# Performance work log

Measured on AMD Instinct MI355X. Metric: run time of the kernel, lower is better.

The kernel has to match this reference:

```python
import jax, jax.numpy as jnp
import numpy as np

B, S, HID = 2, 2048, 2560
H, NOPE, ROPE, VD = 40, 64, 32, 64
QKD = NOPE + ROPE  # 96
Q_RANK, KV_RANK = 768, 256
EPS = 1e-5
SCALING = QKD ** -0.5
NEG = -1e9


def rms_norm(x, w, eps=EPS):
    xf = x.astype(jnp.float32)
    var = jnp.mean(xf * xf, axis=-1, keepdims=True)
    return (xf * jax.lax.rsqrt(var + eps)).astype(x.dtype) * w


def rotate_half(x):
    x1, x2 = jnp.split(x, 2, axis=-1)
    return jnp.concatenate([-x2, x1], axis=-1)


def setup_inputs() -> dict:
    key = jax.random.key(0)
    ks = jax.random.split(key, 8)
    # rotary tables (rope_theta = 10000), shape [S, ROPE]
    inv_freq = 1.0 / (10000.0 ** (np.arange(0, ROPE, 2, dtype=np.float32) / ROPE))
    t = np.arange(S, dtype=np.float32)
    freqs = np.outer(t, inv_freq)  # [S, ROPE/2]
    emb = np.concatenate([freqs, freqs], axis=-1)
    return {
        "hidden_states": jax.random.normal(ks[0], (B, S, HID), jnp.float32),
        "cos": jnp.asarray(np.cos(emb)),
        "sin": jnp.asarray(np.sin(emb)),
        "wq_a": jax.random.normal(ks[1], (HID, Q_RANK), jnp.float32) * 0.02,
        "q_a_ln_w": jnp.ones((Q_RANK,), jnp.float32),
        "wq_b": jax.random.normal(ks[2], (Q_RANK, H * QKD), jnp.float32) * 0.02,
        "wkv_a": jax.random.normal(ks[3], (HID, KV_RANK + ROPE), jnp.float32) * 0.02,
        "kv_a_ln_w": jnp.ones((KV_RANK,), jnp.float32),
        "wkv_b": jax.random.normal(ks[4], (KV_RANK, H * (NOPE + VD)), jnp.float32) * 0.02,
        "wo": jax.random.normal(ks[5], (H * VD, HID), jnp.float32) * 0.02,
    }


def reference(hidden_states, cos, sin, wq_a, q_a_ln_w, wq_b, wkv_a, kv_a_ln_w, wkv_b, wo):
    b, s, _ = hidden_states.shape
    # low-rank query: down-proj, RMSNorm, up-proj
    q = rms_norm(hidden_states @ wq_a, q_a_ln_w) @ wq_b  # [B,S,H*QKD]
    q = q.reshape(b, s, H, QKD).transpose(0, 2, 1, 3)  # [B,H,S,QKD]
    q_pass, q_rot = q[..., :NOPE], q[..., NOPE:]
    # compressed kv + shared rope key
    ckv = hidden_states @ wkv_a  # [B,S,KV_RANK+ROPE]
    k_c, k_rot = ckv[..., :KV_RANK], ckv[..., KV_RANK:]
    kv = rms_norm(k_c, kv_a_ln_w) @ wkv_b  # [B,S,H*(NOPE+VD)]
    kv = kv.reshape(b, s, H, NOPE + VD).transpose(0, 2, 1, 3)  # [B,H,S,NOPE+VD]
    k_pass, v = kv[..., :NOPE], kv[..., NOPE:]
    # partial RoPE (standard rotate-half), cos/sin: [S,ROPE] -> [1,1,S,ROPE]
    c = cos[None, None, :, :]
    si = sin[None, None, :, :]
    q_rot = q_rot * c + rotate_half(q_rot) * si  # [B,H,S,ROPE]
    k_rot = k_rot[:, None, :, :]  # [B,1,S,ROPE]
    k_rot = k_rot * c + rotate_half(k_rot) * si
    k_rot = jnp.broadcast_to(k_rot, (b, H, s, ROPE))
    query = jnp.concatenate([q_pass, q_rot], axis=-1)  # [B,H,S,QKD]
    key = jnp.concatenate([k_pass, k_rot], axis=-1)  # [B,H,S,QKD]
    # eager causal SDPA
    scores = jnp.einsum('bhqd,bhkd->bhqk', query, key) * SCALING
    causal = jnp.tril(jnp.ones((s, s), bool))
    scores = jnp.where(causal[None, None], scores, NEG)
    probs = jax.nn.softmax(scores.astype(jnp.float32), axis=-1).astype(query.dtype)
    out = jnp.einsum('bhqk,bhkd->bhqd', probs, v)  # [B,H,S,VD]
    out = out.transpose(0, 2, 1, 3).reshape(b, s, H * VD)
    return out @ wo
```

## Files before the change

### kernel.cpp

```cpp
#include <hip/hip_runtime.h>
#include <hip/hip_bf16.h>
#include <cstdint>

#define B_ 2
#define S_ 2048
#define HID_ 2560
#define H_ 40
#define NOPE_ 64
#define ROPE_ 32
#define VD_ 64
#define QKD_ 96
#define QRANK_ 768
#define KVRANK_ 256
#define KVRP_ 288
#define KVRP_PAD 384
#define HQKD (H_*QKD_)
#define HKV  (H_*(NOPE_+VD_))
#define HVD  (H_*VD_)
#define TOK  (B_*S_)
#define EPS_ 1e-5f
#define SCALING_ 0.10206207261596575f

typedef __bf16  bf16x8  __attribute__((ext_vector_type(8)));
typedef float   floatx4 __attribute__((ext_vector_type(4)));
typedef short   shortx4 __attribute__((ext_vector_type(4)));
typedef unsigned short ushort8_t __attribute__((ext_vector_type(8)));

__device__ __forceinline__ unsigned short f2bf(float f) {
    unsigned int u = __builtin_bit_cast(unsigned int, f);
    unsigned int r = (u + 0x7FFFu + ((u >> 16) & 1u)) >> 16;
    return (unsigned short)r;
}
__device__ __forceinline__ float bf2f(unsigned short h) {
    return __builtin_bit_cast(float, ((unsigned int)h) << 16);
}
__device__ __forceinline__ float load_in(const void* p, long i, int bf) {
    if (bf) return bf2f(((const unsigned short*)p)[i]);
    return ((const float*)p)[i];
}

__global__ void k_detect(const unsigned short* cosb, int* flag) {
    if (threadIdx.x == 0) flag[0] = (cosb[0] != 0) ? 1 : 0;
}

__global__ void k_tobf(const void* in, unsigned short* out, long n, const int* flag) {
    int bf = flag[0];
    long i = (long)blockIdx.x * blockDim.x + threadIdx.x;
    if (i >= n) return;
    out[i] = bf ? ((const unsigned short*)in)[i] : f2bf(((const float*)in)[i]);
}

__global__ __launch_bounds__(256) void k_transpose(const void* in, unsigned short* out,
                                                   int K, int N, int Npad, const int* flag) {
    __shared__ float tile[32][33];
    int bf = flag[0];
    int k0 = blockIdx.x * 32;
    int n0 = blockIdx.y * 32;
    int tx = threadIdx.x & 31, ty = threadIdx.x >> 5;
#pragma unroll
    for (int i = 0; i < 4; i++) {
        int k = k0 + ty + 8 * i, n = n0 + tx;
        float v = 0.f;
        if (n < N && k < K) v = load_in(in, (long)k * N + n, bf);
        tile[ty + 8 * i][tx] = v;
    }
    __syncthreads();
#pragma unroll
    for (int i = 0; i < 4; i++) {
        int n = n0 + ty + 8 * i, k = k0 + tx;
        if (n < Npad && k < K) out[(long)n * K + k] = f2bf(tile[tx][ty + 8 * i]);
    }
}

__global__ __launch_bounds__(256) void k_vtrans(const unsigned short* kv, unsigned short* vt) {
    __shared__ unsigned short t[32][33];
    int bh = blockIdx.z;
    int s0 = blockIdx.x * 32, v0 = blockIdx.y * 32;
    int b = bh / H_, h = bh % H_;
    int tx = threadIdx.x & 31, ty = threadIdx.x >> 5;
#pragma unroll
    for (int i = 0; i < 4; i++) {
        int s = s0 + ty + 8 * i, vd = v0 + tx;
        t[ty + 8 * i][tx] = kv[((long)b * S_ + s) * HKV + h * 128 + 64 + vd];
    }
    __syncthreads();
#pragma unroll
    for (int i = 0; i < 4; i++) {
        int vd = v0 + ty + 8 * i, s = s0 + tx;
        vt[((long)bh * 64 + vd) * S_ + s] = t[tx][ty + 8 * i];
    }
}

__global__ __launch_bounds__(256) void k_rmsnorm(const float* in, int ldin, int L,
                                                 const void* w, unsigned short* out,
                                                 int ldout, const int* flag) {
    int bf = flag[0];
    long row = blockIdx.x;
    const float* x = in + row * ldin;
    float ss = 0.f;
    for (int i = threadIdx.x; i < L; i += 256) { float v = x[i]; ss += v * v; }
    __shared__ float red[256];
    red[threadIdx.x] = ss;
    __syncthreads();
    for (int s = 128; s > 0; s >>= 1) {
        if (threadIdx.x < s) red[threadIdx.x] += red[threadIdx.x + s];
        __syncthreads();
    }
    float scale = rsqrtf(red[0] / (float)L + EPS_);
    for (int i = threadIdx.x; i < L; i += 256)
        out[row * ldout + i] = f2bf(x[i] * scale * load_in(w, i, bf));
}

__global__ void k_rope_q(unsigned short* q, const void* cosb, const void* sinb, const int* flag) {
    int bf = flag[0];
    long i = (long)blockIdx.x * blockDim.x + threadIdx.x;
    if (i >= (long)TOK * H_ * 16) return;
    int r = (int)(i & 15);
    long t = i >> 4;
    int h = (int)(t % H_);
    long tok = t / H_;
    int s = (int)(tok % S_);
    long base = tok * HQKD + h * QKD_ + NOPE_;
    float x1 = bf2f(q[base + r]), x2 = bf2f(q[base + 16 + r]);
    float c1 = load_in(cosb, (long)s * ROPE_ + r, bf);
    float s1 = load_in(sinb, (long)s * ROPE_ + r, bf);
    float c2 = load_in(cosb, (long)s * ROPE_ + 16 + r, bf);
    float s2 = load_in(sinb, (long)s * ROPE_ + 16 + r, bf);
    q[base + r]      = f2bf(x1 * c1 - x2 * s1);
    q[base + 16 + r] = f2bf(x2 * c2 + x1 * s2);
}

__global__ void k_rope_k(const float* ckv, unsigned short* krot,
                         const void* cosb, const void* sinb, const int* flag) {
    int bf = flag[0];
    long i = (long)blockIdx.x * blockDim.x + threadIdx.x;
    if (i >= (long)TOK * 16) return;
    int r = (int)(i & 15);
    long tok = i >> 4;
    int s = (int)(tok % S_);
    const float* x = ckv + tok * KVRP_PAD + KVRANK_;
    float x1 = x[r], x2 = x[16 + r];
    float c1 = load_in(cosb, (long)s * ROPE_ + r, bf);
    float s1 = load_in(sinb, (long)s * ROPE_ + r, bf);
    float c2 = load_in(cosb, (long)s * ROPE_ + 16 + r, bf);
    float s2 = load_in(sinb, (long)s * ROPE_ + 16 + r, bf);
    krot[tok * ROPE_ + r]      = f2bf(x1 * c1 - x2 * s1);
    krot[tok * ROPE_ + 16 + r] = f2bf(x2 * c2 + x1 * s2);
}

__global__ __launch_bounds__(256) void k_gemm(const unsigned short* A, const unsigned short* Bt,
                                              void* C, int M, int N, int K,
                                              int out_mode, const int* flag) {
    int obf = (out_mode == 2) ? flag[0] : out_mode;
    __shared__ __align__(16) unsigned short As[128][40];
    __shared__ __align__(16) unsigned short Bs[128][40];
    int tid = threadIdx.x;
    int gm = blockIdx.y * 128, gn = blockIdx.x * 128;
    int lane = tid & 63, w = tid >> 6, wm = w >> 1, wn = w & 1;
    int g = lane >> 4, qi = lane & 15;
    floatx4 acc[4][4];
#pragma unroll
    for (int mt = 0; mt < 4; mt++)
#pragma unroll
        for (int nt = 0; nt < 4; nt++) acc[mt][nt] = (floatx4){0.f, 0.f, 0.f, 0.f};

    for (int k0 = 0; k0 < K; k0 += 32) {
        __syncthreads();
#pragma unroll
        for (int i = 0; i < 2; i++) {
            int c = tid + i * 256;
            int row = c >> 2, kc = (c & 3) * 8;
            *(ushort8_t*)&As[row][kc] = *(const ushort8_t*)&A[(long)(gm + row) * K + k0 + kc];
            *(ushort8_t*)&Bs[row][kc] = *(const ushort8_t*)&Bt[(long)(gn + row) * K + k0 + kc];
        }
        __syncthreads();
        bf16x8 fa[4], fb[4];
#pragma unroll
        for (int mt = 0; mt < 4; mt++) fa[mt] = *(const bf16x8*)&As[wm * 64 + mt * 16 + qi][g * 8];
#pragma unroll
        for (int nt = 0; nt < 4; nt++) fb[nt] = *(const bf16x8*)&Bs[wn * 64 + nt * 16 + qi][g * 8];
#pragma unroll
        for (int mt = 0; mt < 4; mt++)
#pragma unroll
            for (int nt = 0; nt < 4; nt++)
                acc[mt][nt] = __builtin_amdgcn_mfma_f32_16x16x32_bf16(fa[mt], fb[nt], acc[mt][nt], 0, 0, 0);
    }
#pragma unroll
    for (int mt = 0; mt < 4; mt++)
#pragma unroll
        for (int nt = 0; nt < 4; nt++)
#pragma unroll
            for (int r = 0; r < 4; r++) {
                long row = gm + wm * 64 + mt * 16 + g * 4 + r;
                long col = gn + wn * 64 + nt * 16 + qi;
                float v = acc[mt][nt][r];
                if (obf) ((unsigned short*)C)[row * N + col] = f2bf(v);
                else     ((float*)C)[row * N + col] = v;
            }
}

__global__ __launch_bounds__(256) void k_attn(const unsigned short* q, const unsigned short* kv,
                                              const unsigned short* krot, const unsigned short* vt,
                                              unsigned short* out) {
    __shared__ __align__(16) unsigned short Ks[64][104];
    __shared__ __align__(16) unsigned short Vs[64][80];
    int tid = threadIdx.x;
    int lane = tid & 63, w = tid >> 6;
    int b = blockIdx.z, h = blockIdx.y;
    int qblk = gridDim.x - 1 - blockIdx.x;
    int g = lane >> 4, qi = lane & 15;
    long tok0 = (long)b * S_;
    int qrow = qblk * 64 + w * 16 + qi;

    const unsigned short* qp = q + (tok0 + qrow) * HQKD + h * QKD_;
    bf16x8 fq[3];
#pragma unroll
    for (int c = 0; c < 3; c++) fq[c] = *(const bf16x8*)&qp[c * 32 + g * 8];

    const unsigned short* kbase = kv + tok0 * HKV + h * 128;
    const unsigned short* vtb = vt + ((long)(b * H_ + h) * 64) * S_;

    floatx4 o[4];
#pragma unroll
    for (int vc = 0; vc < 4; vc++) o[vc] = (floatx4){0.f, 0.f, 0.f, 0.f};
    float m = -1e30f, lsum = 0.f;

    for (int kt = 0; kt <= qblk; kt++) {
        int k0 = kt * 64;
        __syncthreads();
#pragma unroll
        for (int i = 0; i < 2; i++) {
            int idx = tid + i * 256;
            int row = idx >> 3, part = idx & 7;
            *(ushort8_t*)&Ks[row][part * 8] =
                *(const ushort8_t*)&kbase[(long)(k0 + row) * HKV + part * 8];
        }
        {
            int row = tid >> 2, part = tid & 3;
            *(ushort8_t*)&Ks[row][64 + part * 8] =
                *(const ushort8_t*)&krot[(long)(tok0 + k0 + row) * ROPE_ + part * 8];
        }
#pragma unroll
        for (int i = 0; i < 2; i++) {
            int idx = tid + i * 256;
            int row = idx >> 3, part = idx & 7;
            *(ushort8_t*)&Vs[row][part * 8] =
                *(const ushort8_t*)&vtb[(long)row * S_ + k0 + part * 8];
        }
        __syncthreads();

        int kkmax = (kt == qblk) ? w : 3;
        for (int kk = 0; kk <= kkmax; kk++) {
            bf16x8 fk0 = *(const bf16x8*)&Ks[kk * 16 + qi][g * 8];
            bf16x8 fk1 = *(const bf16x8*)&Ks[kk * 16 + qi][32 + g * 8];
            bf16x8 fk2 = *(const bf16x8*)&Ks[kk * 16 + qi][64 + g * 8];
            floatx4 st = (floatx4){0.f, 0.f, 0.f, 0.f};
            st = __builtin_amdgcn_mfma_f32_16x16x32_bf16(fk0, fq[0], st, 0, 0, 0);
            st = __builtin_amdgcn_mfma_f32_16x16x32_bf16(fk1, fq[1], st, 0, 0, 0);
            st = __builtin_amdgcn_mfma_f32_16x16x32_bf16(fk2, fq[2], st, 0, 0, 0);
            bool diag = (kt == qblk) && (kk == w);
            float sv[4], tmax = -3e30f;
#pragma unroll
            for (int r = 0; r < 4; r++) {
                float s = st[r] * SCALING_;
                if (diag && (g * 4 + r) > qi) s = -1e30f;
                sv[r] = s;
                tmax = fmaxf(tmax, s);
            }
            tmax = fmaxf(tmax, __shfl_xor(tmax, 16, 64));
            tmax = fmaxf(tmax, __shfl_xor(tmax, 32, 64));
            float mnew = fmaxf(m, tmax);
            float alpha = __expf(m - mnew);
            float ps = 0.f;
            shortx4 fp;
#pragma unroll
            for (int r = 0; r < 4; r++) {
                float p = __expf(sv[r] - mnew);
                ps += p;
                fp[r] = (short)f2bf(p);
            }
            ps += __shfl_xor(ps, 16, 64);
            ps += __shfl_xor(ps, 32, 64);
            lsum = lsum * alpha + ps;
            m = mnew;
            float ar[4];
#pragma unroll
            for (int r = 0; r < 4; r++) ar[r] = __shfl(alpha, (lane & 48) | (g * 4 + r), 64);
#pragma unroll
            for (int vc = 0; vc < 4; vc++) {
                o[vc][0] *= ar[0]; o[vc][1] *= ar[1]; o[vc][2] *= ar[2]; o[vc][3] *= ar[3];
            }
#pragma unroll
            for (int vc = 0; vc < 4; vc++) {
                shortx4 fv = *(const shortx4*)&Vs[vc * 16 + qi][kk * 16 + g * 4];
                o[vc] = __builtin_amdgcn_mfma_f32_16x16x16bf16_1k(fp, fv, o[vc], 0, 0, 0);
            }
        }
    }
    float lr[4];
#pragma unroll
    for (int r = 0; r < 4; r++) lr[r] = __shfl(lsum, (lane & 48) | (g * 4 + r), 64);
#pragma unroll
    for (int vc = 0; vc < 4; vc++)
#pragma unroll
        for (int r = 0; r < 4; r++)
            out[(tok0 + qblk * 64 + w * 16 + g * 4 + r) * HVD + h * VD_ + vc * 16 + qi] =
                f2bf(o[vc][r] / lr[r]);
}

extern "C" void kernel_launch(void* const* d_in, const int* in_sizes, int n_in,
                              void* d_out, int out_size, void* d_ws, size_t ws_size,
                              hipStream_t stream) {
    const void* hidden = d_in[0];
    const void* cosb   = d_in[1];
    const void* sinb   = d_in[2];
    const void* wq_a   = d_in[3];
    const void* q_ln   = d_in[4];
    const void* wq_b   = d_in[5];
    const void* wkv_a  = d_in[6];
    const void* kv_ln  = d_in[7];
    const void* wkv_b  = d_in[8];
    const void* wo     = d_in[9];

    char* ws = (char*)d_ws;
    size_t off = 0;
    auto alloc = [&](size_t bytes) -> void* {
        void* p = ws + off;
        off += (bytes + 255) & ~(size_t)255;
        return p;
    };
    int* flag                = (int*)alloc(256);
    unsigned short* hbf      = (unsigned short*)alloc((size_t)TOK * HID_ * 2);
    unsigned short* wqa_t    = (unsigned short*)alloc((size_t)QRANK_ * HID_ * 2);
    unsigned short* wqb_t    = (unsigned short*)alloc((size_t)HQKD * QRANK_ * 2);
    unsigned short* wkva_t   = (unsigned short*)alloc((size_t)KVRP_PAD * HID_ * 2);
    unsigned short* wkvb_t   = (unsigned short*)alloc((size_t)HKV * KVRANK_ * 2);
    unsigned short* wo_t     = (unsigned short*)alloc((size_t)HID_ * HVD * 2);
    float*          q_a      = (float*)alloc((size_t)TOK * QRANK_ * 4);
    unsigned short* q_a_n    = (unsigned short*)alloc((size_t)TOK * QRANK_ * 2);
    unsigned short* q_raw    = (unsigned short*)alloc((size_t)TOK * HQKD * 2);
    float*          ckv      = (float*)alloc((size_t)TOK * KVRP_PAD * 4);
    unsigned short* kc_n     = (unsigned short*)alloc((size_t)TOK * KVRANK_ * 2);
    unsigned short* kv_raw   = (unsigned short*)alloc((size_t)TOK * HKV * 2);
    unsigned short* krot     = (unsigned short*)alloc((size_t)TOK * ROPE_ * 2);
    unsigned short* attn_o   = (unsigned short*)alloc((size_t)TOK * HVD * 2);
    unsigned short* vt       = hbf;

    k_detect<<<1, 64, 0, stream>>>((const unsigned short*)cosb, flag);

    long nh = (long)TOK * HID_;
    k_tobf<<<(int)((nh + 255) / 256), 256, 0, stream>>>(hidden, hbf, nh, flag);

    k_transpose<<<dim3(HID_ / 32, QRANK_ / 32), 256, 0, stream>>>(wq_a, wqa_t, HID_, QRANK_, QRANK_, flag);
    k_transpose<<<dim3(QRANK_ / 32, HQKD / 32), 256, 0, stream>>>(wq_b, wqb_t, QRANK_, HQKD, HQKD, flag);
    k_transpose<<<dim3(HID_ / 32, KVRP_PAD / 32), 256, 0, stream>>>(wkv_a, wkva_t, HID_, KVRP_, KVRP_PAD, flag);
    k_transpose<<<dim3(KVRANK_ / 32, HKV / 32), 256, 0, stream>>>(wkv_b, wkvb_t, KVRANK_, HKV, HKV, flag);
    k_transpose<<<dim3(HVD / 32, HID_ / 32), 256, 0, stream>>>(wo, wo_t, HVD, HID_, HID_, flag);

    k_gemm<<<dim3(QRANK_ / 128, TOK / 128), 256, 0, stream>>>(hbf, wqa_t, q_a, TOK, QRANK_, HID_, 0, flag);
    k_rmsnorm<<<TOK, 256, 0, stream>>>(q_a, QRANK_, QRANK_, q_ln, q_a_n, QRANK_, flag);
    k_gemm<<<dim3(HQKD / 128, TOK / 128), 256, 0, stream>>>(q_a_n, wqb_t, q_raw, TOK, HQKD, QRANK_, 1, flag);

    k_gemm<<<dim3(KVRP_PAD / 128, TOK / 128), 256, 0, stream>>>(hbf, wkva_t, ckv, TOK, KVRP_PAD, HID_, 0, flag);
    k_rmsnorm<<<TOK, 256, 0, stream>>>(ckv, KVRP_PAD, KVRANK_, kv_ln, kc_n, KVRANK_, flag);
    k_gemm<<<dim3(HKV / 128, TOK / 128), 256, 0, stream>>>(kc_n, wkvb_t, kv_raw, TOK, HKV, KVRANK_, 1, flag);

    long nrq = (long)TOK * H_ * 16;
    k_rope_q<<<(int)((nrq + 255) / 256), 256, 0, stream>>>(q_raw, cosb, sinb, flag);
    long nrk = (long)TOK * 16;
    k_rope_k<<<(int)((nrk + 255) / 256), 256, 0, stream>>>(ckv, krot, cosb, sinb, flag);

    k_vtrans<<<dim3(S_ / 32, VD_ / 32, B_ * H_), 256, 0, stream>>>(kv_raw, vt);
    k_attn<<<dim3(S_ / 64, H_, B_), 256, 0, stream>>>(q_raw, kv_raw, krot, vt, attn_o);

    k_gemm<<<dim3(HID_ / 128, TOK / 128), 256, 0, stream>>>(attn_o, wo_t, d_out, TOK, HID_, HVD, 2, flag);
}
```

Measured before the change: 873.4 us.

## Use direct global-to-LDS loads in GEMM and 128-row query tiles in attention

The GEMM now stages A/B tiles with global_load_lds 16-byte direct copies into unpadded LDS, which removes the register round-trip but introduces LDS bank conflicts because the row padding is gone. The attention kernel now handles 128 query rows per block, with each wave owning 32 rows as two 16-row tiles. This reuses each K/V tile loaded into LDS across twice as many queries and batches the QK MFMAs for a whole 64-key tile before the softmax. The cost is more registers per wave, fewer blocks, and coarser causal masking, with waves skipping the tiles past their diagonal.

```diff
diff --git a/kernel.cpp b/kernel.cpp
--- a/kernel.cpp
+++ b/kernel.cpp
@@ -39,6 +39,12 @@
     return ((const float*)p)[i];
 }
 
+__device__ __forceinline__ void gl_lds16(const unsigned short* g, unsigned short* l) {
+    __builtin_amdgcn_global_load_lds(
+        (const __attribute__((address_space(1))) unsigned int*)g,
+        (__attribute__((address_space(3))) unsigned int*)l, 16, 0, 0);
+}
+
 __global__ void k_detect(const unsigned short* cosb, int* flag) {
     if (threadIdx.x == 0) flag[0] = (cosb[0] != 0) ? 1 : 0;
 }
@@ -152,12 +158,23 @@
                                               void* C, int M, int N, int K,
                                               int out_mode, const int* flag) {
     int obf = (out_mode == 2) ? flag[0] : out_mode;
-    __shared__ __align__(16) unsigned short As[128][40];
-    __shared__ __align__(16) unsigned short Bs[128][40];
+    __shared__ __align__(16) unsigned short As[128 * 32];
+    __shared__ __align__(16) unsigned short Bs[128 * 32];
     int tid = threadIdx.x;
     int gm = blockIdx.y * 128, gn = blockIdx.x * 128;
     int lane = tid & 63, w = tid >> 6, wm = w >> 1, wn = w & 1;
     int g = lane >> 4, qi = lane & 15;
+    int srow = lane >> 2;
+    int scol = (lane & 3) * 8;
+    const unsigned short* Ag0 = A  + (long)(gm + w * 16 + srow) * K + scol;
+    const unsigned short* Ag1 = A  + (long)(gm + (w + 4) * 16 + srow) * K + scol;
+    const unsigned short* Bg0 = Bt + (long)(gn + w * 16 + srow) * K + scol;
+    const unsigned short* Bg1 = Bt + (long)(gn + (w + 4) * 16 + srow) * K + scol;
+    unsigned short* Al0 = &As[w * 512];
+    unsigned short* Al1 = &As[(w + 4) * 512];
+    unsigned short* Bl0 = &Bs[w * 512];
+    unsigned short* Bl1 = &Bs[(w + 4) * 512];
+
     floatx4 acc[4][4];
 #pragma unroll
     for (int mt = 0; mt < 4; mt++)
@@ -166,19 +183,16 @@
 
     for (int k0 = 0; k0 < K; k0 += 32) {
         __syncthreads();
-#pragma unroll
-        for (int i = 0; i < 2; i++) {
-            int c = tid + i * 256;
-            int row = c >> 2, kc = (c & 3) * 8;
-            *(ushort8_t*)&As[row][kc] = *(const ushort8_t*)&A[(long)(gm + row) * K + k0 + kc];
-            *(ushort8_t*)&Bs[row][kc] = *(const ushort8_t*)&Bt[(long)(gn + row) * K + k0 + kc];
-        }
+        gl_lds16(Ag0 + k0, Al0);
+        gl_lds16(Ag1 + k0, Al1);
+        gl_lds16(Bg0 + k0, Bl0);
+        gl_lds16(Bg1 + k0, Bl1);
         __syncthreads();
         bf16x8 fa[4], fb[4];
 #pragma unroll
-        for (int mt = 0; mt < 4; mt++) fa[mt] = *(const bf16x8*)&As[wm * 64 + mt * 16 + qi][g * 8];
-#pragma unroll
-        for (int nt = 0; nt < 4; nt++) fb[nt] = *(const bf16x8*)&Bs[wn * 64 + nt * 16 + qi][g * 8];
+        for (int mt = 0; mt < 4; mt++) fa[mt] = *(const bf16x8*)&As[(wm * 64 + mt * 16 + qi) * 32 + g * 8];
+#pragma unroll
+        for (int nt = 0; nt < 4; nt++) fb[nt] = *(const bf16x8*)&Bs[(wn * 64 + nt * 16 + qi) * 32 + g * 8];
 #pragma unroll
         for (int mt = 0; mt < 4; mt++)
 #pragma unroll
@@ -202,110 +216,145 @@
 __global__ __launch_bounds__(256) void k_attn(const unsigned short* q, const unsigned short* kv,
                                               const unsigned short* krot, const unsigned short* vt,
                                               unsigned short* out) {
-    __shared__ __align__(16) unsigned short Ks[64][104];
-    __shared__ __align__(16) unsigned short Vs[64][80];
+    __shared__ __align__(16) unsigned short Ks[64 * 96];
+    __shared__ __align__(16) unsigned short Vs[64 * 80];
     int tid = threadIdx.x;
     int lane = tid & 63, w = tid >> 6;
     int b = blockIdx.z, h = blockIdx.y;
     int qblk = gridDim.x - 1 - blockIdx.x;
+    int qbase = qblk * 128;
     int g = lane >> 4, qi = lane & 15;
     long tok0 = (long)b * S_;
-    int qrow = qblk * 64 + w * 16 + qi;
-
-    const unsigned short* qp = q + (tok0 + qrow) * HQKD + h * QKD_;
-    bf16x8 fq[3];
-#pragma unroll
-    for (int c = 0; c < 3; c++) fq[c] = *(const bf16x8*)&qp[c * 32 + g * 8];
+
+    bf16x8 fq[2][3];
+#pragma unroll
+    for (int qt = 0; qt < 2; qt++) {
+        const unsigned short* qp = q + (tok0 + qbase + w * 32 + qt * 16 + qi) * HQKD + h * QKD_;
+#pragma unroll
+        for (int c = 0; c < 3; c++) fq[qt][c] = *(const bf16x8*)&qp[c * 32 + g * 8];
+    }
 
     const unsigned short* kbase = kv + tok0 * HKV + h * 128;
-    const unsigned short* vtb = vt + ((long)(b * H_ + h) * 64) * S_;
-
-    floatx4 o[4];
-#pragma unroll
-    for (int vc = 0; vc < 4; vc++) o[vc] = (floatx4){0.f, 0.f, 0.f, 0.f};
-    float m = -1e30f, lsum = 0.f;
-
-    for (int kt = 0; kt <= qblk; kt++) {
+    const unsigned short* krb   = krot + tok0 * ROPE_;
+    const unsigned short* vtb   = vt + ((long)(b * H_ + h) * 64) * S_;
+
+    floatx4 o[2][4];
+#pragma unroll
+    for (int qt = 0; qt < 2; qt++)
+#pragma unroll
+        for (int vc = 0; vc < 4; vc++) o[qt][vc] = (floatx4){0.f, 0.f, 0.f, 0.f};
+    float m[2] = {-1e30f, -1e30f}, l[2] = {0.f, 0.f};
+
+    int ktb = 2 * qblk + 2;
+    int ktmax_w = (qbase + w * 32 + 31) >> 6;
+
+    for (int kt = 0; kt < ktb; kt++) {
         int k0 = kt * 64;
         __syncthreads();
 #pragma unroll
+        for (int i = 0; i < 3; i++) {
+            int idx = tid + i * 256;
+            int row = idx / 12, c = (idx % 12) * 8;
+            const unsigned short* src = (c < 64)
+                ? kbase + (long)(k0 + row) * HKV + c
+                : krb + (long)(k0 + row) * ROPE_ + (c - 64);
+            *(ushort8_t*)&Ks[row * 96 + c] = *(const ushort8_t*)src;
+        }
+#pragma unroll
         for (int i = 0; i < 2; i++) {
             int idx = tid + i * 256;
-            int row = idx >> 3, part = idx & 7;
-            *(ushort8_t*)&Ks[row][part * 8] =
-                *(const ushort8_t*)&kbase[(long)(k0 + row) * HKV + part * 8];
-        }
-        {
-            int row = tid >> 2, part = tid & 3;
-            *(ushort8_t*)&Ks[row][64 + part * 8] =
-                *(const ushort8_t*)&krot[(long)(tok0 + k0 + row) * ROPE_ + part * 8];
-        }
-#pragma unroll
-        for (int i = 0; i < 2; i++) {
-            int idx = tid + i * 256;
-            int row = idx >> 3, part = idx & 7;
-            *(ushort8_t*)&Vs[row][part * 8] =
-                *(const ushort8_t*)&vtb[(long)row * S_ + k0 + part * 8];
+            int row = idx >> 3, c = (idx & 7) * 8;
+            *(ushort8_t*)&Vs[row * 80 + c] = *(const ushort8_t*)&vtb[(long)row * S_ + k0 + c];
         }
         __syncthreads();
-
-        int kkmax = (kt == qblk) ? w : 3;
-        for (int kk = 0; kk <= kkmax; kk++) {
-            bf16x8 fk0 = *(const bf16x8*)&Ks[kk * 16 + qi][g * 8];
-            bf16x8 fk1 = *(const bf16x8*)&Ks[kk * 16 + qi][32 + g * 8];
-            bf16x8 fk2 = *(const bf16x8*)&Ks[kk * 16 + qi][64 + g * 8];
-            floatx4 st = (floatx4){0.f, 0.f, 0.f, 0.f};
-            st = __builtin_amdgcn_mfma_f32_16x16x32_bf16(fk0, fq[0], st, 0, 0, 0);
-            st = __builtin_amdgcn_mfma_f32_16x16x32_bf16(fk1, fq[1], st, 0, 0, 0);
-            st = __builtin_amdgcn_mfma_f32_16x16x32_bf16(fk2, fq[2], st, 0, 0, 0);
-            bool diag = (kt == qblk) && (kk == w);
-            float sv[4], tmax = -3e30f;
-#pragma unroll
-            for (int r = 0; r < 4; r++) {
-                float s = st[r] * SCALING_;
-                if (diag && (g * 4 + r) > qi) s = -1e30f;
-                sv[r] = s;
-                tmax = fmaxf(tmax, s);
+        if (kt > ktmax_w) continue;
+
+        floatx4 st[2][4];
+#pragma unroll
+        for (int kk = 0; kk < 4; kk++) {
+            const unsigned short* kr = &Ks[(kk * 16 + qi) * 96];
+            bf16x8 fk0 = *(const bf16x8*)&kr[g * 8];
+            bf16x8 fk1 = *(const bf16x8*)&kr[32 + g * 8];
+            bf16x8 fk2 = *(const bf16x8*)&kr[64 + g * 8];
+#pragma unroll
+            for (int qt = 0; qt < 2; qt++) {
+                floatx4 s = (floatx4){0.f, 0.f, 0.f, 0.f};
+                s = __builtin_amdgcn_mfma_f32_16x16x32_bf16(fk0, fq[qt][0], s, 0, 0, 0);
+                s = __builtin_amdgcn_mfma_f32_16x16x32_bf16(fk1, fq[qt][1], s, 0, 0, 0);
+                s = __builtin_amdgcn_mfma_f32_16x16x32_bf16(fk2, fq[qt][2], s, 0, 0, 0);
+                st[qt][kk] = s;
             }
+        }
+
+        shortx4 fp[2][4];
+#pragma unroll
+        for (int qt = 0; qt < 2; qt++) {
+            int qrow = qbase + w * 32 + qt * 16 + qi;
+            bool need_mask = (k0 + 63) > (qbase + w * 32 + qt * 16);
+            float sv[4][4];
+            float tmax = -3e30f;
+#pragma unroll
+            for (int kk = 0; kk < 4; kk++)
+#pragma unroll
+                for (int r = 0; r < 4; r++) {
+                    float s = st[qt][kk][r] * SCALING_;
+                    if (need_mask && (k0 + kk * 16 + g * 4 + r) > qrow) s = -1e30f;
+                    sv[kk][r] = s;
+                    tmax = fmaxf(tmax, s);
+                }
             tmax = fmaxf(tmax, __shfl_xor(tmax, 16, 64));
             tmax = fmaxf(tmax, __shfl_xor(tmax, 32, 64));
-            float mnew = fmaxf(m, tmax);
-            float alpha = __expf(m - mnew);
+            float mnew = fmaxf(m[qt], tmax);
+            float alpha = __expf(m[qt] - mnew);
             float ps = 0.f;
-            shortx4 fp;
-#pragma unroll
-            for (int r = 0; r < 4; r++) {
-                float p = __expf(sv[r] - mnew);
-                ps += p;
-                fp[r] = (short)f2bf(p);
-            }
+#pragma unroll
+            for (int kk = 0; kk < 4; kk++)
+#pragma unroll
+                for (int r = 0; r < 4; r++) {
+                    float p = __expf(sv[kk][r] - mnew);
+                    ps += p;
+                    fp[qt][kk][r] = (short)f2bf(p);
+                }
             ps += __shfl_xor(ps, 16, 64);
             ps += __shfl_xor(ps, 32, 64);
-            lsum = lsum * alpha + ps;
-            m = mnew;
+            l[qt] = l[qt] * alpha + ps;
+            m[qt] = mnew;
             float ar[4];
 #pragma unroll
             for (int r = 0; r < 4; r++) ar[r] = __shfl(alpha, (lane & 48) | (g * 4 + r), 64);
 #pragma unroll
             for (int vc = 0; vc < 4; vc++) {
-                o[vc][0] *= ar[0]; o[vc][1] *= ar[1]; o[vc][2] *= ar[2]; o[vc][3] *= ar[3];
-            }
-#pragma unroll
-            for (int vc = 0; vc < 4; vc++) {
-                shortx4 fv = *(const shortx4*)&Vs[vc * 16 + qi][kk * 16 + g * 4];
-                o[vc] = __builtin_amdgcn_mfma_f32_16x16x16bf16_1k(fp, fv, o[vc], 0, 0, 0);
+                o[qt][vc][0] *= ar[0]; o[qt][vc][1] *= ar[1];
+                o[qt][vc][2] *= ar[2]; o[qt][vc][3] *= ar[3];
             }
         }
-    }
-    float lr[4];
-#pragma unroll
-    for (int r = 0; r < 4; r++) lr[r] = __shfl(lsum, (lane & 48) | (g * 4 + r), 64);
-#pragma unroll
-    for (int vc = 0; vc < 4; vc++)
-#pragma unroll
-        for (int r = 0; r < 4; r++)
-            out[(tok0 + qblk * 64 + w * 16 + g * 4 + r) * HVD + h * VD_ + vc * 16 + qi] =
-                f2bf(o[vc][r] / lr[r]);
+
+#pragma unroll
+        for (int kk = 0; kk < 4; kk++) {
+            shortx4 fv[4];
+#pragma unroll
+            for (int vc = 0; vc < 4; vc++)
+                fv[vc] = *(const shortx4*)&Vs[(vc * 16 + qi) * 80 + kk * 16 + g * 4];
+#pragma unroll
+            for (int qt = 0; qt < 2; qt++)
+#pragma unroll
+                for (int vc = 0; vc < 4; vc++)
+                    o[qt][vc] = __builtin_amdgcn_mfma_f32_16x16x16bf16_1k(fp[qt][kk], fv[vc], o[qt][vc], 0, 0, 0);
+        }
+    }
+
+#pragma unroll
+    for (int qt = 0; qt < 2; qt++) {
+        float lr[4];
+#pragma unroll
+        for (int r = 0; r < 4; r++) lr[r] = __shfl(l[qt], (lane & 48) | (g * 4 + r), 64);
+#pragma unroll
+        for (int vc = 0; vc < 4; vc++)
+#pragma unroll
+            for (int r = 0; r < 4; r++)
+                out[(tok0 + qbase + w * 32 + qt * 16 + g * 4 + r) * HVD + h * VD_ + vc * 16 + qi] =
+                    f2bf(o[qt][vc][r] / lr[r]);
+    }
 }
 
 extern "C" void kernel_launch(void* const* d_in, const int* in_sizes, int n_in,
@@ -371,7 +420,7 @@
     k_rope_k<<<(int)((nrk + 255) / 256), 256, 0, stream>>>(ckv, krot, cosb, sinb, flag);
 
     k_vtrans<<<dim3(S_ / 32, VD_ / 32, B_ * H_), 256, 0, stream>>>(kv_raw, vt);
-    k_attn<<<dim3(S_ / 64, H_, B_), 256, 0, stream>>>(q_raw, kv_raw, krot, vt, attn_o);
+    k_attn<<<dim3(S_ / 128, H_, B_), 256, 0, stream>>>(q_raw, kv_raw, krot, vt, attn_o);
 
     k_gemm<<<dim3(HID_ / 128, TOK / 128), 256, 0, stream>>>(attn_o, wo_t, d_out, TOK, HID_, HVD, 2, flag);
 }
```

After: 812.0 us. 7.0% less time.
